# Kernel optimization log

Measured on AMD Instinct MI355X. Metric: run time of the kernel, lower is better.

## Reference

```python
import jax, jax.numpy as jnp
import numpy as np

N_HEAD = 8
HEAD_HIDDEN = 16
NODE_HIDDEN = 128
EDGE_HIDDEN = 64


def setup_inputs() -> dict:
    key = jax.random.key(0)
    ks = jax.random.split(key, 12)
    b, n = 2, 512
    hd = N_HEAD * HEAD_HIDDEN
    s = 0.05
    x = jax.random.normal(ks[0], (b, n, NODE_HIDDEN), dtype=jnp.float32)
    edge_attr = jax.random.normal(ks[1], (b, n, n, EDGE_HIDDEN), dtype=jnp.float32)
    mask = jax.random.randint(ks[2], (b, n), 0, 2) > 0
    Wqkv = jax.random.normal(ks[3], (NODE_HIDDEN, 3 * hd), dtype=jnp.float32) * s
    bqkv = jax.random.normal(ks[4], (3 * hd,), dtype=jnp.float32) * s
    We = jax.random.normal(ks[5], (EDGE_HIDDEN, hd), dtype=jnp.float32) * s
    be = jax.random.normal(ks[6], (hd,), dtype=jnp.float32) * s
    Wno = jax.random.normal(ks[7], (hd, NODE_HIDDEN), dtype=jnp.float32) * s
    bno = jax.random.normal(ks[8], (NODE_HIDDEN,), dtype=jnp.float32) * s
    Weo = jax.random.normal(ks[9], (hd, EDGE_HIDDEN), dtype=jnp.float32) * s
    beo = jax.random.normal(ks[10], (EDGE_HIDDEN,), dtype=jnp.float32) * s
    return {"x": x, "edge_attr": edge_attr, "mask": mask,
            "Wqkv": Wqkv, "bqkv": bqkv, "We": We, "be": be,
            "Wno": Wno, "bno": bno, "Weo": Weo, "beo": beo}


def reference(x, edge_attr, mask, Wqkv, bqkv, We, be, Wno, bno, Weo, beo):
    b, n, _ = x.shape
    h, d = N_HEAD, HEAD_HIDDEN
    qkv = x @ Wqkv + bqkv                      # b n 3hd
    q, k, v = jnp.split(qkv, 3, axis=-1)
    e = edge_attr @ We + be                    # b i j (h d)
    q = q.reshape(b, n, 1, h, d)               # b i 1 h d
    k = k.reshape(b, 1, n, h, d)               # b 1 j h d
    v = v.reshape(b, n, h, d)                  # b j h d
    e = e.reshape(b, n, n, h, d)               # b i j h d
    raw_att = q * k * e                        # b i j h d (reused for edge_out)
    att = raw_att.sum(axis=-1) / np.float32(np.sqrt(d))  # b i j h
    neg = -jnp.finfo(att.dtype).max
    att = jnp.where(mask[:, None, :, None], att, neg)
    att = jax.nn.softmax(att, axis=-2)         # softmax over j
    node = jnp.einsum('bijh,bjhd->bihd', att, v).reshape(b, n, h * d)
    node_out = node @ Wno + bno
    edge_out = raw_att.reshape(b, n, n, h * d) @ Weo + beo
    return node_out, edge_out
```

## Files before the change

### kernel.cpp

```cpp
#include <hip/hip_runtime.h>
#include <hip/hip_bf16.h>
#include <stdint.h>

#define NN 512
#define HD 128

typedef __attribute__((ext_vector_type(8))) short bf16x8;
typedef __attribute__((ext_vector_type(4))) float f32x4;

static __device__ __forceinline__ float bf2f(unsigned short u) {
  union { uint32_t u32; float f; } cv; cv.u32 = ((uint32_t)u) << 16; return cv.f;
}
static __device__ __forceinline__ unsigned short f2bf(float f) {
  union { float f; uint32_t u; } cv; cv.f = f;
  return (unsigned short)((cv.u + 0x7FFFu + ((cv.u >> 16) & 1u)) >> 16);
}

struct DetectArgs { const uint16_t* p[10]; int n[10]; };

__global__ __launch_bounds__(256) void detect_kernel(DetectArgs a, int* __restrict__ flags) {
  __shared__ int acc[256];
  const int ti = blockIdx.x;
  int n = a.n[ti]; if (n > 2048) n = 2048;
  int g = 0;
  for (int w = threadIdx.x; w < n; w += 256) {
    uint16_t v = a.p[ti][w];
    int e = (v >> 7) & 0xFF;
    g += (v == 0u || (e >= 90 && e <= 133)) ? 1 : 0;
  }
  acc[threadIdx.x] = g;
  __syncthreads();
  for (int s = 128; s > 0; s >>= 1) {
    if (threadIdx.x < s) acc[threadIdx.x] += acc[threadIdx.x + s];
    __syncthreads();
  }
  if (threadIdx.x == 0) flags[ti] = (acc[0] * 10 < n * 9) ? 1 : 0;
}

__global__ __launch_bounds__(256) void mask_bias_kernel(const uint32_t* __restrict__ raw,
                                                        float* __restrict__ mbias, int count) {
  int inspect = count >> 2; if (inspect > 256) inspect = 256;
  bool ok_i32 = true, ok_f32 = true, ok_bf16 = true;
  #pragma unroll 1
  for (int w = 0; w < inspect; ++w) {
    uint32_t v = raw[w];
    if (v > 1u) ok_i32 = false;
    if (!(v == 0u || v == 0x3F800000u)) ok_f32 = false;
    uint32_t lo = v & 0xFFFFu, hi = v >> 16;
    if (!((lo == 0u || lo == 0x3F80u) && (hi == 0u || hi == 0x3F80u))) ok_bf16 = false;
  }
  int idx = blockIdx.x * 256 + threadIdx.x;
  if (idx < count) {
    bool on;
    if (ok_i32 || ok_f32) on = raw[idx] != 0u;
    else if (ok_bf16)     on = ((const uint16_t*)raw)[idx] != 0u;
    else                  on = ((const uint8_t*)raw)[idx] != 0u;
    mbias[idx] = on ? 0.0f : -1e30f;
  }
}

__global__ __launch_bounds__(128) void qkv_kernel(const void* __restrict__ xp,
                                                  const void* __restrict__ Wp,
                                                  const void* __restrict__ bp,
                                                  const int* __restrict__ flags,
                                                  uint16_t* __restrict__ qf,
                                                  uint16_t* __restrict__ kf,
                                                  uint16_t* __restrict__ vf) {
  const int f_x = flags[0], f_W = flags[2], f_b = flags[3];
  const int row = blockIdx.x;
  const int t = threadIdx.x;
  __shared__ float xs[HD];
  xs[t] = f_x ? ((const float*)xp)[row * HD + t] : bf2f(((const uint16_t*)xp)[row * HD + t]);
  __syncthreads();
  float aq = 0.f, ak = 0.f, av = 0.f;
  if (f_W) {
    const float* W = (const float*)Wp;
    #pragma unroll 4
    for (int kk = 0; kk < HD; ++kk) {
      float xv = xs[kk]; const float* wr = W + kk * 384;
      aq = fmaf(xv, wr[t], aq);
      ak = fmaf(xv, wr[128 + t], ak);
      av = fmaf(xv, wr[256 + t], av);
    }
  } else {
    const uint16_t* W = (const uint16_t*)Wp;
    #pragma unroll 4
    for (int kk = 0; kk < HD; ++kk) {
      float xv = xs[kk]; const uint16_t* wr = W + kk * 384;
      aq = fmaf(xv, bf2f(wr[t]), aq);
      ak = fmaf(xv, bf2f(wr[128 + t]), ak);
      av = fmaf(xv, bf2f(wr[256 + t]), av);
    }
  }
  float bq = f_b ? ((const float*)bp)[t]       : bf2f(((const uint16_t*)bp)[t]);
  float bk = f_b ? ((const float*)bp)[128 + t] : bf2f(((const uint16_t*)bp)[128 + t]);
  float bv = f_b ? ((const float*)bp)[256 + t] : bf2f(((const uint16_t*)bp)[256 + t]);
  qf[row * HD + t] = f2bf(aq + bq);
  kf[row * HD + ((t & 15) << 3) + (t >> 4)] = f2bf(ak + bk);
  vf[((size_t)((row >> 9) * HD + t)) * NN + (row & (NN - 1))] = f2bf(av + bv);
}

__global__ __launch_bounds__(512, 4) void gat_main_kernel(
    const void* __restrict__ eap,
    const void* __restrict__ Wep,  const void* __restrict__ bep,
    const void* __restrict__ Wnop, const void* __restrict__ bnop,
    const void* __restrict__ Weop, const void* __restrict__ beop,
    const int* __restrict__ flags,
    const uint16_t* __restrict__ qf, const uint16_t* __restrict__ kf,
    const uint16_t* __restrict__ vf, const float* __restrict__ mbias,
    float* __restrict__ node_out, float* __restrict__ edge_out) {
  const int tid = threadIdx.x;
  const int w = tid >> 6, lane = tid & 63;
  const int l15 = lane & 15, quad = lane >> 4;
  const int bb = blockIdx.x >> 9;
  const int i  = blockIdx.x & (NN - 1);
  const int f_ea = flags[1], f_We = flags[4], f_be = flags[5];
  const int f_Wno = flags[6], f_bno = flags[7], f_Weo = flags[8], f_beo = flags[9];

  __shared__ __align__(16) uint16_t B1f[8 * 2 * 64 * 8];
  __shared__ __align__(16) uint16_t B2f[5 * 4 * 64 * 8];
  __shared__ __align__(16) uint16_t raw_s[8 * 16 * 136];
  __shared__ __align__(16) uint16_t att_s[8 * NN];
  __shared__ __align__(16) float q_s[HD];
  __shared__ __align__(16) float beq_s[HD];
  __shared__ __align__(16) float beo_s[64];
  __shared__ __align__(16) float node_s[HD];

  if (tid < HD) q_s[tid] = bf2f(qf[(bb * NN + i) * HD + tid]);
  if (tid >= 128 && tid < 192) {
    int c = tid - 128;
    beo_s[c] = f_beo ? ((const float*)beop)[c] : bf2f(((const uint16_t*)beop)[c]);
  }
  __syncthreads();

  if (tid < HD) {
    float b = f_be ? ((const float*)bep)[tid] : bf2f(((const uint16_t*)bep)[tid]);
    beq_s[tid] = b * q_s[tid];
  }
  for (int slot = tid; slot < 1024; slot += 512) {
    const int t = slot >> 7, s = (slot >> 6) & 1, ln = slot & 63;
    const int c = t * 16 + (ln & 15);
    const int k0 = s * 32 + (ln >> 4) * 8;
    const float qc = q_s[c];
    bf16x8 fr;
    if (f_We) {
      const float* W = (const float*)Wep;
      #pragma unroll
      for (int e = 0; e < 8; ++e) fr[e] = (short)f2bf(W[(k0 + e) * HD + c] * qc);
    } else {
      const uint16_t* W = (const uint16_t*)Wep;
      #pragma unroll
      for (int e = 0; e < 8; ++e) fr[e] = (short)f2bf(bf2f(W[(k0 + e) * HD + c]) * qc);
    }
    *(bf16x8*)&B1f[slot * 8] = fr;
  }
  for (int slot = tid; slot < 1280; slot += 512) {
    const int t2 = slot >> 8, s = (slot >> 6) & 3, ln = slot & 63;
    bf16x8 fr;
    if (t2 == 4) {
      const int head = s * 2 + ((ln >> 5) & 1);
      const short v = ((ln & 15) == head) ? (short)0x3F80 : (short)0;
      #pragma unroll
      for (int e = 0; e < 8; ++e) fr[e] = v;
    } else {
      const int c = t2 * 16 + (ln & 15);
      const int k0 = s * 32 + ((ln >> 4) & 3) * 8;
      if (f_Weo) {
        const float* W = (const float*)Weop;
        #pragma unroll
        for (int e = 0; e < 8; ++e) fr[e] = (short)f2bf(W[(k0 + e) * 64 + c]);
      } else {
        const uint16_t* W = (const uint16_t*)Weop;
        #pragma unroll
        for (int e = 0; e < 8; ++e) fr[e] = (short)W[(k0 + e) * 64 + c];
      }
    }
    *(bf16x8*)&B2f[slot * 8] = fr;
  }
  __syncthreads();

  const size_t io_base = (size_t)(bb * NN + i) * NN * 64;
  const uint16_t* kperm = kf + (size_t)bb * NN * HD;
  const float* mrow = mbias + bb * NN;
  uint16_t* rws = raw_s + w * (16 * 136);
  float*    fws = (float*)rws;

  auto body = [&](int band, const bf16x8* A1) {
    const int j0 = band * 16;
    const f32x4 mr = *(const f32x4*)(mrow + j0 + quad * 4);
    bf16x8 k8[4];
    #pragma unroll
    for (int r = 0; r < 4; ++r)
      k8[r] = *(const bf16x8*)(kperm + (size_t)(j0 + quad * 4 + r) * HD + l15 * 8);

    #pragma unroll
    for (int t = 0; t < 8; ++t) {
      const float bv = beq_s[t * 16 + l15];
      f32x4 a = {bv, bv, bv, bv};
      a = __builtin_amdgcn_mfma_f32_16x16x32_bf16(
            A1[0], *(const bf16x8*)&B1f[(t * 2 + 0) * 512 + lane * 8], a, 0, 0, 0);
      a = __builtin_amdgcn_mfma_f32_16x16x32_bf16(
            A1[1], *(const bf16x8*)&B1f[(t * 2 + 1) * 512 + lane * 8], a, 0, 0, 0);
      #pragma unroll
      for (int r = 0; r < 4; ++r)
        rws[(quad * 4 + r) * 136 + t * 16 + l15] =
            f2bf(a[r] * bf2f((unsigned short)k8[r][t]));
    }

    bf16x8 A2[4];
    #pragma unroll
    for (int s = 0; s < 4; ++s)
      A2[s] = *(const bf16x8*)&rws[l15 * 136 + s * 32 + quad * 8];

    {
      f32x4 aL = {0.f, 0.f, 0.f, 0.f};
      #pragma unroll
      for (int s = 0; s < 4; ++s)
        aL = __builtin_amdgcn_mfma_f32_16x16x32_bf16(
               A2[s], *(const bf16x8*)&B2f[(16 + s) * 512 + lane * 8], aL, 0, 0, 0);
      if (l15 < 8) {
        att_s[l15 * NN + (j0 + quad * 4 + 0)] = f2bf(aL[0] * 0.25f + mr[0]);
        att_s[l15 * NN + (j0 + quad * 4 + 1)] = f2bf(aL[1] * 0.25f + mr[1]);
        att_s[l15 * NN + (j0 + quad * 4 + 2)] = f2bf(aL[2] * 0.25f + mr[2]);
        att_s[l15 * NN + (j0 + quad * 4 + 3)] = f2bf(aL[3] * 0.25f + mr[3]);
      }
    }

    #pragma unroll
    for (int t2 = 0; t2 < 4; ++t2) {
      const float bv = beo_s[t2 * 16 + l15];
      f32x4 a2 = {bv, bv, bv, bv};
      #pragma unroll
      for (int s = 0; s < 4; ++s)
        a2 = __builtin_amdgcn_mfma_f32_16x16x32_bf16(
               A2[s], *(const bf16x8*)&B2f[(t2 * 4 + s) * 512 + lane * 8], a2, 0, 0, 0);
      #pragma unroll
      for (int r = 0; r < 4; ++r)
        fws[(quad * 4 + r) * 68 + t2 * 16 + l15] = a2[r];
    }

    float* eo = edge_out + io_base + (size_t)j0 * 64;
    #pragma unroll
    for (int u = 0; u < 4; ++u) {
      const int jr = u * 4 + quad;
      f32x4 vv = *(const f32x4*)&fws[jr * 68 + l15 * 4];
      __builtin_nontemporal_store(vv, (f32x4*)(eo + jr * 64) + l15);
    }
  };

  if (f_ea) {
    f32x4 ef[4];
    {
      const float* ea = (const float*)eap + io_base + (size_t)(w * 16 + l15) * 64 + quad * 8;
      ef[0] = __builtin_nontemporal_load((const f32x4*)ea);
      ef[1] = __builtin_nontemporal_load((const f32x4*)(ea + 4));
      ef[2] = __builtin_nontemporal_load((const f32x4*)(ea + 32));
      ef[3] = __builtin_nontemporal_load((const f32x4*)(ea + 36));
    }
    #pragma unroll
    for (int bi = 0; bi < 4; ++bi) {
      const int band = w + bi * 8;
      f32x4 efn[4];
      if (bi < 3) {
        const float* ea = (const float*)eap + io_base + (size_t)((band + 8) * 16 + l15) * 64 + quad * 8;
        efn[0] = __builtin_nontemporal_load((const f32x4*)ea);
        efn[1] = __builtin_nontemporal_load((const f32x4*)(ea + 4));
        efn[2] = __builtin_nontemporal_load((const f32x4*)(ea + 32));
        efn[3] = __builtin_nontemporal_load((const f32x4*)(ea + 36));
      }
      bf16x8 A1[2];
      #pragma unroll
      for (int s = 0; s < 2; ++s) {
        bf16x8 a;
        #pragma unroll
        for (int e = 0; e < 4; ++e) {
          a[e]     = (short)f2bf(ef[2 * s][e]);
          a[e + 4] = (short)f2bf(ef[2 * s + 1][e]);
        }
        A1[s] = a;
      }
      body(band, A1);
      if (bi < 3) {
        #pragma unroll
        for (int s = 0; s < 4; ++s) ef[s] = efn[s];
      }
    }
  } else {
    bf16x8 eb[2];
    {
      const uint16_t* ea = (const uint16_t*)eap + io_base + (size_t)(w * 16 + l15) * 64 + quad * 8;
      eb[0] = __builtin_nontemporal_load((const bf16x8*)ea);
      eb[1] = __builtin_nontemporal_load((const bf16x8*)(ea + 32));
    }
    #pragma unroll
    for (int bi = 0; bi < 4; ++bi) {
      const int band = w + bi * 8;
      bf16x8 ebn[2];
      if (bi < 3) {
        const uint16_t* ea = (const uint16_t*)eap + io_base + (size_t)((band + 8) * 16 + l15) * 64 + quad * 8;
        ebn[0] = __builtin_nontemporal_load((const bf16x8*)ea);
        ebn[1] = __builtin_nontemporal_load((const bf16x8*)(ea + 32));
      }
      body(band, eb);
      if (bi < 3) { eb[0] = ebn[0]; eb[1] = ebn[1]; }
    }
  }
  __syncthreads();

  {
    float vals[8];
    float m = -3.4e38f;
    #pragma unroll
    for (int it = 0; it < 8; ++it)
      m = fmaxf(m, bf2f(att_s[w * NN + it * 64 + lane]));
    #pragma unroll
    for (int off = 32; off; off >>= 1) m = fmaxf(m, __shfl_xor(m, off));
    float ssum = 0.f;
    #pragma unroll
    for (int it = 0; it < 8; ++it) {
      float v = __expf(bf2f(att_s[w * NN + it * 64 + lane]) - m);
      vals[it] = v; ssum += v;
    }
    #pragma unroll
    for (int off = 32; off; off >>= 1) ssum += __shfl_xor(ssum, off);
    const float inv = 1.0f / ssum;
    #pragma unroll
    for (int it = 0; it < 8; ++it)
      att_s[w * NN + it * 64 + lane] = f2bf(vals[it] * inv);
  }

  {
    const int c = w * 16 + l15;
    const uint16_t* vb = vf + ((size_t)(bb * HD + c)) * NN + quad * 128;
    float acc = 0.f;
    #pragma unroll
    for (int u = 0; u < 16; ++u) {
      bf16x8 v8 = *(const bf16x8*)(vb + u * 8);
      bf16x8 a8 = *(const bf16x8*)&att_s[w * NN + quad * 128 + u * 8];
      #pragma unroll
      for (int e = 0; e < 8; ++e)
        acc = fmaf(bf2f((unsigned short)a8[e]), bf2f((unsigned short)v8[e]), acc);
    }
    acc += __shfl_xor(acc, 16);
    acc += __shfl_xor(acc, 32);
    if (quad == 0) node_s[c] = acc;
  }
  __syncthreads();

  if (tid < HD) {
    float acc = f_bno ? ((const float*)bnop)[tid] : bf2f(((const uint16_t*)bnop)[tid]);
    if (f_Wno) {
      const float* W = (const float*)Wnop;
      #pragma unroll 4
      for (int kk = 0; kk < HD; ++kk) acc = fmaf(node_s[kk], W[kk * HD + tid], acc);
    } else {
      const uint16_t* W = (const uint16_t*)Wnop;
      #pragma unroll 4
      for (int kk = 0; kk < HD; ++kk) acc = fmaf(node_s[kk], bf2f(W[kk * HD + tid]), acc);
    }
    node_out[(bb * NN + i) * HD + tid] = acc;
  }
}

extern "C" void kernel_launch(void* const* d_in, const int* in_sizes, int n_in,
                              void* d_out, int out_size, void* d_ws, size_t ws_size,
                              hipStream_t stream) {
  const int b = in_sizes[0] / (NN * HD);
  const int rows = b * NN;

  int*   flags = (int*)d_ws;
  float* mbias = (float*)((char*)d_ws + 64);
  uint16_t* qf = (uint16_t*)((char*)d_ws + 64 + 4096);
  uint16_t* kf = qf + (size_t)rows * HD;
  uint16_t* vf = kf + (size_t)rows * HD;

  float* node_out = (float*)d_out;
  float* edge_out = node_out + (size_t)rows * HD;

  DetectArgs da;
  const int float_idx[10] = {0, 1, 3, 4, 5, 6, 7, 8, 9, 10};
  for (int t = 0; t < 10; ++t) {
    da.p[t] = (const uint16_t*)d_in[float_idx[t]];
    da.n[t] = in_sizes[float_idx[t]];
  }

  detect_kernel<<<10, 256, 0, stream>>>(da, flags);
  mask_bias_kernel<<<(rows + 255) / 256, 256, 0, stream>>>((const uint32_t*)d_in[2], mbias, rows);
  qkv_kernel<<<rows, 128, 0, stream>>>(d_in[0], d_in[3], d_in[4], flags, qf, kf, vf);
  gat_main_kernel<<<rows, 512, 0, stream>>>(d_in[1], d_in[5], d_in[6], d_in[7], d_in[8],
                                            d_in[9], d_in[10], flags,
                                            qf, kf, vf, mbias, node_out, edge_out);
}
```

Measured before the change: 355.0 us.

## Hold weight fragments in registers, shrink LDS, and use MFMA for attention-V

New measurement: 712.2 us. 101% more time.

```diff
diff --git a/kernel.cpp b/kernel.cpp
--- a/kernel.cpp
+++ b/kernel.cpp
@@ -14,6 +14,11 @@
 static __device__ __forceinline__ unsigned short f2bf(float f) {
   union { float f; uint32_t u; } cv; cv.f = f;
   return (unsigned short)((cv.u + 0x7FFFu + ((cv.u >> 16) & 1u)) >> 16);
+}
+static __device__ __forceinline__ uint32_t cvtpk(float lo, float hi) {
+  uint32_t r;
+  asm("v_cvt_pk_bf16_f32 %0, %1, %2" : "=v"(r) : "v"(lo), "v"(hi));
+  return r;
 }
 
 struct DetectArgs { const uint16_t* p[10]; int n[10]; };
@@ -100,7 +105,7 @@
   vf[((size_t)((row >> 9) * HD + t)) * NN + (row & (NN - 1))] = f2bf(av + bv);
 }
 
-__global__ __launch_bounds__(512, 4) void gat_main_kernel(
+__global__ __launch_bounds__(512, 6) void gat_main_kernel(
     const void* __restrict__ eap,
     const void* __restrict__ Wep,  const void* __restrict__ bep,
     const void* __restrict__ Wnop, const void* __restrict__ bnop,
@@ -117,10 +122,9 @@
   const int f_ea = flags[1], f_We = flags[4], f_be = flags[5];
   const int f_Wno = flags[6], f_bno = flags[7], f_Weo = flags[8], f_beo = flags[9];
 
-  __shared__ __align__(16) uint16_t B1f[8 * 2 * 64 * 8];
-  __shared__ __align__(16) uint16_t B2f[5 * 4 * 64 * 8];
-  __shared__ __align__(16) uint16_t raw_s[8 * 16 * 136];
-  __shared__ __align__(16) uint16_t att_s[8 * NN];
+  __shared__ __align__(16) uint16_t pool[10240];
+  __shared__ __align__(16) uint16_t BLf[4 * 64 * 8];
+  __shared__ __align__(16) uint16_t att_s[8 * 520];
   __shared__ __align__(16) float q_s[HD];
   __shared__ __align__(16) float beq_s[HD];
   __shared__ __align__(16) float beo_s[64];
@@ -130,6 +134,15 @@
   if (tid >= 128 && tid < 192) {
     int c = tid - 128;
     beo_s[c] = f_beo ? ((const float*)beop)[c] : bf2f(((const uint16_t*)beop)[c]);
+  }
+  if (tid < 256) {
+    const int s = tid >> 6, ln = tid & 63;
+    const int head = s * 2 + ((ln >> 5) & 1);
+    const short v = ((ln & 15) == head) ? (short)0x3F80 : (short)0;
+    bf16x8 fr;
+    #pragma unroll
+    for (int e = 0; e < 8; ++e) fr[e] = v;
+    *(bf16x8*)&BLf[(s * 64 + ln) * 8] = fr;
   }
   __syncthreads();
 
@@ -152,37 +165,44 @@
       #pragma unroll
       for (int e = 0; e < 8; ++e) fr[e] = (short)f2bf(bf2f(W[(k0 + e) * HD + c]) * qc);
     }
-    *(bf16x8*)&B1f[slot * 8] = fr;
-  }
-  for (int slot = tid; slot < 1280; slot += 512) {
+    *(bf16x8*)&pool[slot * 8] = fr;
+  }
+  __syncthreads();
+  bf16x8 B1r[16];
+  #pragma unroll
+  for (int f = 0; f < 16; ++f) B1r[f] = *(const bf16x8*)&pool[(f * 64 + lane) * 8];
+  float beq_r[8], beo_r[4];
+  #pragma unroll
+  for (int t = 0; t < 8; ++t) beq_r[t] = beq_s[t * 16 + l15];
+  #pragma unroll
+  for (int t2 = 0; t2 < 4; ++t2) beo_r[t2] = beo_s[t2 * 16 + l15];
+  __syncthreads();
+  for (int slot = tid; slot < 1024; slot += 512) {
     const int t2 = slot >> 8, s = (slot >> 6) & 3, ln = slot & 63;
+    const int c = t2 * 16 + (ln & 15);
+    const int k0 = s * 32 + ((ln >> 4) & 3) * 8;
     bf16x8 fr;
-    if (t2 == 4) {
-      const int head = s * 2 + ((ln >> 5) & 1);
-      const short v = ((ln & 15) == head) ? (short)0x3F80 : (short)0;
-      #pragma unroll
-      for (int e = 0; e < 8; ++e) fr[e] = v;
+    if (f_Weo) {
+      const float* W = (const float*)Weop;
+      #pragma unroll
+      for (int e = 0; e < 8; ++e) fr[e] = (short)f2bf(W[(k0 + e) * 64 + c]);
     } else {
-      const int c = t2 * 16 + (ln & 15);
-      const int k0 = s * 32 + ((ln >> 4) & 3) * 8;
-      if (f_Weo) {
-        const float* W = (const float*)Weop;
-        #pragma unroll
-        for (int e = 0; e < 8; ++e) fr[e] = (short)f2bf(W[(k0 + e) * 64 + c]);
-      } else {
-        const uint16_t* W = (const uint16_t*)Weop;
-        #pragma unroll
-        for (int e = 0; e < 8; ++e) fr[e] = (short)W[(k0 + e) * 64 + c];
-      }
-    }
-    *(bf16x8*)&B2f[slot * 8] = fr;
-  }
+      const uint16_t* W = (const uint16_t*)Weop;
+      #pragma unroll
+      for (int e = 0; e < 8; ++e) fr[e] = (short)W[(k0 + e) * 64 + c];
+    }
+    *(bf16x8*)&pool[slot * 8] = fr;
+  }
+  __syncthreads();
+  bf16x8 B2r[16];
+  #pragma unroll
+  for (int f = 0; f < 16; ++f) B2r[f] = *(const bf16x8*)&pool[(f * 64 + lane) * 8];
   __syncthreads();
 
   const size_t io_base = (size_t)(bb * NN + i) * NN * 64;
   const uint16_t* kperm = kf + (size_t)bb * NN * HD;
   const float* mrow = mbias + bb * NN;
-  uint16_t* rws = raw_s + w * (16 * 136);
+  uint16_t* rws = pool + w * 1152;
   float*    fws = (float*)rws;
 
   auto body = [&](int band, const bf16x8* A1) {
@@ -193,58 +213,68 @@
     for (int r = 0; r < 4; ++r)
       k8[r] = *(const bf16x8*)(kperm + (size_t)(j0 + quad * 4 + r) * HD + l15 * 8);
 
-    #pragma unroll
-    for (int t = 0; t < 8; ++t) {
-      const float bv = beq_s[t * 16 + l15];
-      f32x4 a = {bv, bv, bv, bv};
-      a = __builtin_amdgcn_mfma_f32_16x16x32_bf16(
-            A1[0], *(const bf16x8*)&B1f[(t * 2 + 0) * 512 + lane * 8], a, 0, 0, 0);
-      a = __builtin_amdgcn_mfma_f32_16x16x32_bf16(
-            A1[1], *(const bf16x8*)&B1f[(t * 2 + 1) * 512 + lane * 8], a, 0, 0, 0);
+    f32x4 acc2[4];
+    #pragma unroll
+    for (int t2 = 0; t2 < 4; ++t2) {
+      const float bv = beo_r[t2];
+      acc2[t2] = (f32x4){bv, bv, bv, bv};
+    }
+    f32x4 aL = {0.f, 0.f, 0.f, 0.f};
+
+    #pragma unroll
+    for (int h = 0; h < 2; ++h) {
+      #pragma unroll
+      for (int tl = 0; tl < 4; ++tl) {
+        const int t = h * 4 + tl;
+        const float bv = beq_r[t];
+        f32x4 a = {bv, bv, bv, bv};
+        a = __builtin_amdgcn_mfma_f32_16x16x32_bf16(A1[0], B1r[t * 2 + 0], a, 0, 0, 0);
+        a = __builtin_amdgcn_mfma_f32_16x16x32_bf16(A1[1], B1r[t * 2 + 1], a, 0, 0, 0);
+        const float v0 = a[0] * bf2f((unsigned short)k8[0][t]);
+        const float v1 = a[1] * bf2f((unsigned short)k8[1][t]);
+        const float v2 = a[2] * bf2f((unsigned short)k8[2][t]);
+        const float v3 = a[3] * bf2f((unsigned short)k8[3][t]);
+        const uint32_t p01 = cvtpk(v0, v1), p23 = cvtpk(v2, v3);
+        uint16_t* rp = &rws[(tl ^ quad) * 16 + l15];
+        rp[(quad * 4 + 0) * 72] = (uint16_t)p01;
+        rp[(quad * 4 + 1) * 72] = (uint16_t)(p01 >> 16);
+        rp[(quad * 4 + 2) * 72] = (uint16_t)p23;
+        rp[(quad * 4 + 3) * 72] = (uint16_t)(p23 >> 16);
+      }
+      #pragma unroll
+      for (int sl = 0; sl < 2; ++sl) {
+        const int s = h * 2 + sl;
+        const int blk = (sl * 2 + (quad >> 1)) ^ (l15 >> 2);
+        const bf16x8 A2 = *(const bf16x8*)&rws[l15 * 72 + blk * 16 + (quad & 1) * 8];
+        aL = __builtin_amdgcn_mfma_f32_16x16x32_bf16(A2, *(const bf16x8*)&BLf[(s * 64 + lane) * 8], aL, 0, 0, 0);
+        #pragma unroll
+        for (int t2 = 0; t2 < 4; ++t2)
+          acc2[t2] = __builtin_amdgcn_mfma_f32_16x16x32_bf16(A2, B2r[t2 * 4 + s], acc2[t2], 0, 0, 0);
+      }
+    }
+
+    if (l15 < 8) {
       #pragma unroll
       for (int r = 0; r < 4; ++r)
-        rws[(quad * 4 + r) * 136 + t * 16 + l15] =
-            f2bf(a[r] * bf2f((unsigned short)k8[r][t]));
-    }
-
-    bf16x8 A2[4];
-    #pragma unroll
-    for (int s = 0; s < 4; ++s)
-      A2[s] = *(const bf16x8*)&rws[l15 * 136 + s * 32 + quad * 8];
-
-    {
-      f32x4 aL = {0.f, 0.f, 0.f, 0.f};
-      #pragma unroll
-      for (int s = 0; s < 4; ++s)
-        aL = __builtin_amdgcn_mfma_f32_16x16x32_bf16(
-               A2[s], *(const bf16x8*)&B2f[(16 + s) * 512 + lane * 8], aL, 0, 0, 0);
-      if (l15 < 8) {
-        att_s[l15 * NN + (j0 + quad * 4 + 0)] = f2bf(aL[0] * 0.25f + mr[0]);
-        att_s[l15 * NN + (j0 + quad * 4 + 1)] = f2bf(aL[1] * 0.25f + mr[1]);
-        att_s[l15 * NN + (j0 + quad * 4 + 2)] = f2bf(aL[2] * 0.25f + mr[2]);
-        att_s[l15 * NN + (j0 + quad * 4 + 3)] = f2bf(aL[3] * 0.25f + mr[3]);
-      }
-    }
-
-    #pragma unroll
-    for (int t2 = 0; t2 < 4; ++t2) {
-      const float bv = beo_s[t2 * 16 + l15];
-      f32x4 a2 = {bv, bv, bv, bv};
-      #pragma unroll
-      for (int s = 0; s < 4; ++s)
-        a2 = __builtin_amdgcn_mfma_f32_16x16x32_bf16(
-               A2[s], *(const bf16x8*)&B2f[(t2 * 4 + s) * 512 + lane * 8], a2, 0, 0, 0);
-      #pragma unroll
-      for (int r = 0; r < 4; ++r)
-        fws[(quad * 4 + r) * 68 + t2 * 16 + l15] = a2[r];
-    }
-
-    float* eo = edge_out + io_base + (size_t)j0 * 64;
-    #pragma unroll
-    for (int u = 0; u < 4; ++u) {
-      const int jr = u * 4 + quad;
-      f32x4 vv = *(const f32x4*)&fws[jr * 68 + l15 * 4];
-      __builtin_nontemporal_store(vv, (f32x4*)(eo + jr * 64) + l15);
+        att_s[l15 * 520 + (j0 + quad * 4 + r)] = f2bf(aL[r] * 0.25f + mr[r]);
+    }
+
+    #pragma unroll
+    for (int ch = 0; ch < 2; ++ch) {
+      #pragma unroll
+      for (int t2l = 0; t2l < 2; ++t2l) {
+        const int t2 = ch * 2 + t2l;
+        #pragma unroll
+        for (int r = 0; r < 4; ++r)
+          fws[(quad * 4 + r) * 36 + t2l * 16 + l15] = acc2[t2][r];
+      }
+      #pragma unroll
+      for (int rg = 0; rg < 2; ++rg) {
+        const int row = rg * 8 + (lane >> 3);
+        f32x4 vv = *(const f32x4*)&fws[row * 36 + (lane & 7) * 4];
+        __builtin_nontemporal_store(vv,
+            (f32x4*)(edge_out + io_base + (size_t)(j0 + row) * 64 + ch * 32) + (lane & 7));
+      }
     }
   };
 
@@ -271,13 +301,12 @@
       bf16x8 A1[2];
       #pragma unroll
       for (int s = 0; s < 2; ++s) {
-        bf16x8 a;
-        #pragma unroll
-        for (int e = 0; e < 4; ++e) {
-          a[e]     = (short)f2bf(ef[2 * s][e]);
-          a[e + 4] = (short)f2bf(ef[2 * s + 1][e]);
-        }
-        A1[s] = a;
+        union { bf16x8 v; uint32_t u[4]; } cv;
+        cv.u[0] = cvtpk(ef[2 * s][0], ef[2 * s][1]);
+        cv.u[1] = cvtpk(ef[2 * s][2], ef[2 * s][3]);
+        cv.u[2] = cvtpk(ef[2 * s + 1][0], ef[2 * s + 1][1]);
+        cv.u[3] = cvtpk(ef[2 * s + 1][2], ef[2 * s + 1][3]);
+        A1[s] = cv.v;
       }
       body(band, A1);
       if (bi < 3) {
@@ -312,13 +341,13 @@
     float m = -3.4e38f;
     #pragma unroll
     for (int it = 0; it < 8; ++it)
-      m = fmaxf(m, bf2f(att_s[w * NN + it * 64 + lane]));
+      m = fmaxf(m, bf2f(att_s[w * 520 + it * 64 + lane]));
     #pragma unroll
     for (int off = 32; off; off >>= 1) m = fmaxf(m, __shfl_xor(m, off));
     float ssum = 0.f;
     #pragma unroll
     for (int it = 0; it < 8; ++it) {
-      float v = __expf(bf2f(att_s[w * NN + it * 64 + lane]) - m);
+      float v = __expf(bf2f(att_s[w * 520 + it * 64 + lane]) - m);
       vals[it] = v; ssum += v;
     }
     #pragma unroll
@@ -326,39 +355,61 @@
     const float inv = 1.0f / ssum;
     #pragma unroll
     for (int it = 0; it < 8; ++it)
-      att_s[w * NN + it * 64 + lane] = f2bf(vals[it] * inv);
-  }
+      att_s[w * 520 + it * 64 + lane] = f2bf(vals[it] * inv);
+  }
+  __syncthreads();
 
   {
-    const int c = w * 16 + l15;
-    const uint16_t* vb = vf + ((size_t)(bb * HD + c)) * NN + quad * 128;
+    f32x4 nacc[8];
+    #pragma unroll
+    for (int t = 0; t < 8; ++t) nacc[t] = (f32x4){0.f, 0.f, 0.f, 0.f};
+    const uint16_t* vbase = vf + (size_t)bb * HD * NN;
+    #pragma unroll
+    for (int ks = 0; ks < 2; ++ks) {
+      const int k0 = w * 64 + ks * 32;
+      const bf16x8 Af = *(const bf16x8*)&att_s[(l15 & 7) * 520 + k0 + quad * 8];
+      #pragma unroll
+      for (int t = 0; t < 8; ++t) {
+        const bf16x8 Bf = *(const bf16x8*)(vbase + (size_t)(t * 16 + l15) * NN + k0 + quad * 8);
+        nacc[t] = __builtin_amdgcn_mfma_f32_16x16x32_bf16(Af, Bf, nacc[t], 0, 0, 0);
+      }
+    }
+    float* red = (float*)pool;
+    #pragma unroll
+    for (int t = 0; t < 8; ++t)
+      if (quad == (t >> 2)) red[w * 128 + t * 16 + l15] = nacc[t][t & 3];
+    __syncthreads();
+    if (tid < HD) {
+      float s = 0.f;
+      #pragma unroll
+      for (int w2 = 0; w2 < 8; ++w2) s += red[w2 * 128 + tid];
+      node_s[tid] = s;
+    }
+    __syncthreads();
+  }
+
+  {
+    const int c = tid & 127, part = tid >> 7;
     float acc = 0.f;
-    #pragma unroll
-    for (int u = 0; u < 16; ++u) {
-      bf16x8 v8 = *(const bf16x8*)(vb + u * 8);
-      bf16x8 a8 = *(const bf16x8*)&att_s[w * NN + quad * 128 + u * 8];
-      #pragma unroll
-      for (int e = 0; e < 8; ++e)
-        acc = fmaf(bf2f((unsigned short)a8[e]), bf2f((unsigned short)v8[e]), acc);
-    }
-    acc += __shfl_xor(acc, 16);
-    acc += __shfl_xor(acc, 32);
-    if (quad == 0) node_s[c] = acc;
-  }
-  __syncthreads();
-
-  if (tid < HD) {
-    float acc = f_bno ? ((const float*)bnop)[tid] : bf2f(((const uint16_t*)bnop)[tid]);
     if (f_Wno) {
       const float* W = (const float*)Wnop;
-      #pragma unroll 4
-      for (int kk = 0; kk < HD; ++kk) acc = fmaf(node_s[kk], W[kk * HD + tid], acc);
+      #pragma unroll 8
+      for (int kk = part * 32; kk < part * 32 + 32; ++kk)
+        acc = fmaf(node_s[kk], W[kk * HD + c], acc);
     } else {
       const uint16_t* W = (const uint16_t*)Wnop;
-      #pragma unroll 4
-      for (int kk = 0; kk < HD; ++kk) acc = fmaf(node_s[kk], bf2f(W[kk * HD + tid]), acc);
-    }
-    node_out[(bb * NN + i) * HD + tid] = acc;
+      #pragma unroll 8
+      for (int kk = part * 32; kk < part * 32 + 32; ++kk)
+        acc = fmaf(node_s[kk], bf2f(W[kk * HD + c]), acc);
+    }
+    float* red2 = (float*)pool + 1024;
+    red2[tid] = acc;
+    __syncthreads();
+    if (tid < HD) {
+      float b = f_bno ? ((const float*)bnop)[tid] : bf2f(((const uint16_t*)bnop)[tid]);
+      float r = red2[tid] + red2[128 + tid] + red2[256 + tid] + red2[384 + tid] + b;
+      node_out[(bb * NN + i) * HD + tid] = r;
+    }
   }
 }
 
```
